# Kernel tuning notes

Measured on AMD Instinct MI355X. Metric: run time of the kernel, lower is better.

Reference implementation:

```python
import jax, jax.numpy as jnp
import numpy as np

H = 8  # attention_heads


def _ln(x, w, b, eps=1e-5):
    mu = x.mean(axis=-1, keepdims=True)
    var = x.var(axis=-1, keepdims=True)
    return (x - mu) / jnp.sqrt(var + eps) * w + b


def setup_inputs() -> dict:
    key = jax.random.key(0)
    ks = jax.random.split(key, 10)
    B, T, C, U, D, P = 4, 256, 2048, 4, 512, 512
    s = 0.02
    inp = {
        "model_embed": jax.random.normal(ks[0], (B, T, D), jnp.float32),
        "context_embed_key": jax.random.normal(ks[1], (C, U, D), jnp.float32),
        "context_embed_value": jax.random.normal(ks[2], (C, D), jnp.float32),
        "ln1_w": jnp.ones((D,), jnp.float32), "ln1_b": jnp.zeros((D,), jnp.float32),
        "ln2_w": jnp.ones((D,), jnp.float32), "ln2_b": jnp.zeros((D,), jnp.float32),
        "ln3_w": jnp.ones((D,), jnp.float32), "ln3_b": jnp.zeros((D,), jnp.float32),
        "ln4_w": jnp.ones((D,), jnp.float32), "ln4_b": jnp.zeros((D,), jnp.float32),
        "wq": jax.random.normal(ks[3], (D, D), jnp.float32) * s, "bq": jnp.zeros((D,), jnp.float32),
        "wk": jax.random.normal(ks[4], (D, D), jnp.float32) * s, "bk": jnp.zeros((D,), jnp.float32),
        "wv": jax.random.normal(ks[5], (D, D), jnp.float32) * s, "bv": jnp.zeros((D,), jnp.float32),
        "wo": jax.random.normal(ks[6], (D, D), jnp.float32) * s, "bo": jnp.zeros((D,), jnp.float32),
        "wp": jax.random.normal(ks[7], (D, P), jnp.float32) * s, "bp": jnp.zeros((P,), jnp.float32),
    }
    return inp


def reference(model_embed, context_embed_key, context_embed_value,
              ln1_w, ln1_b, ln2_w, ln2_b, ln3_w, ln3_b, ln4_w, ln4_b,
              wq, bq, wk, bk, wv, bv, wo, bo, wp, bp):
    B, T, D = model_embed.shape
    C, U, _ = context_embed_key.shape
    dk = D // H
    # pre-attention LayerNorms (norm_before_x1/x2/x3)
    q = _ln(model_embed, ln1_w, ln1_b)
    k = _ln(context_embed_key, ln2_w, ln2_b)
    v = _ln(context_embed_value, ln3_w, ln3_b)
    # q/k/v projections, split heads
    q = (q @ wq + bq).reshape(B, T, H, dk)
    k = (k @ wk + bk).reshape(C, U, H, dk)
    v = (v @ wv + bv).reshape(C, H, dk)
    # ColBERT late interaction: score every query token against every
    # context vector, MaxSim over the U vectors of each context entry.
    scores = jnp.einsum('bthd,cuhd->bhtcu', q, k) / jnp.sqrt(jnp.asarray(dk, q.dtype))
    scores = scores.max(axis=-1)                 # [B,H,T,C]
    attn = jax.nn.softmax(scores, axis=-1)       # softmax over contexts C
    out = jnp.einsum('bhtc,chd->bthd', attn, v).reshape(B, T, D)
    out = out @ wo + bo                          # attention output proj
    out = _ln(out, ln4_w, ln4_b)                 # norm_after
    return out @ wp + bp                         # final proj -> [B,T,P]
```

## Files before the change

kernel.cpp:

```cpp
#include <hip/hip_runtime.h>
#include <hip/hip_bf16.h>

using bf16 = __hip_bfloat16;

#define D_DIM 512
#define C_DIM 2048
#define U_DIM 4
#define DK 64

typedef __attribute__((ext_vector_type(8))) short short8;
typedef __attribute__((ext_vector_type(8))) unsigned short ushort8;
typedef __attribute__((ext_vector_type(4))) float f32x4;

__device__ __forceinline__ float dload(const void* p, size_t i, int f) {
    return f ? ((const float*)p)[i] : __bfloat162float(((const bf16*)p)[i]);
}
__device__ __forceinline__ unsigned f2bf(float x) {
    bf16 b = __float2bfloat16(x);
    return (unsigned)*(unsigned short*)&b;
}
__device__ __forceinline__ float bf2f(unsigned short us) {
    unsigned u = ((unsigned)us) << 16;
    return __builtin_bit_cast(float, u);
}

__device__ __forceinline__ int block_detect(const void* __restrict__ x) {
    __shared__ int sred[4];
    const bf16* xb = (const bf16*)x;
    int tid = threadIdx.x;
    int cnt = 0;
    #pragma unroll
    for (int i = 0; i < 4; ++i) {
        ushort8 a = *(const ushort8*)(xb + (size_t)(i * 256 + tid) * 8);
        #pragma unroll
        for (int j = 0; j < 8; ++j) {
            float v = fabsf(bf2f(a[j]));
            if (!(v <= 100.0f)) cnt++;
        }
    }
    #pragma unroll
    for (int o = 32; o > 0; o >>= 1) cnt += __shfl_down(cnt, o);
    if ((tid & 63) == 0) sred[tid >> 6] = cnt;
    __syncthreads();
    int c = sred[0] + sred[1] + sred[2] + sred[3];
    return (c > 400) ? 1 : 0;
}

template <bool LN, bool XF, bool WF>
__device__ __forceinline__ void pack_a_body(const void* __restrict__ X,
                                            const void* __restrict__ lnw,
                                            const void* __restrict__ lnb,
                                            uint4* __restrict__ Af, int tt) {
    int m = threadIdx.x >> 4;
    int kbL = threadIdx.x & 15;
    int row = tt * 16 + m;
    float v[32];
    float s = 0.0f, ss = 0.0f;
    #pragma unroll
    for (int i = 0; i < 4; ++i) {
        int k0 = (kbL + i * 16) * 8;
        if constexpr (XF) {
            const float4* p = (const float4*)((const float*)X + (size_t)row * D_DIM + k0);
            float4 a = p[0], b = p[1];
            v[i*8+0] = a.x; v[i*8+1] = a.y; v[i*8+2] = a.z; v[i*8+3] = a.w;
            v[i*8+4] = b.x; v[i*8+5] = b.y; v[i*8+6] = b.z; v[i*8+7] = b.w;
        } else {
            ushort8 a = *(const ushort8*)((const bf16*)X + (size_t)row * D_DIM + k0);
            #pragma unroll
            for (int j = 0; j < 8; ++j) v[i*8+j] = bf2f(a[j]);
        }
        #pragma unroll
        for (int j = 0; j < 8; ++j) { float x = v[i*8+j]; s += x; ss += x * x; }
    }
    float mu = 0.0f, rs = 1.0f;
    if (LN) {
        #pragma unroll
        for (int o = 1; o < 16; o <<= 1) { s += __shfl_xor(s, o); ss += __shfl_xor(ss, o); }
        mu = s * (1.0f / D_DIM);
        float var = ss * (1.0f / D_DIM) - mu * mu;
        rs = rsqrtf(var + 1e-5f);
    }
    #pragma unroll
    for (int i = 0; i < 4; ++i) {
        int kb = kbL + i * 16;
        int k0 = kb * 8;
        float lw[8], lb[8];
        if (LN) {
            if constexpr (WF) {
                const float4* pw = (const float4*)((const float*)lnw + k0);
                const float4* pb = (const float4*)((const float*)lnb + k0);
                float4 w0 = pw[0], w1 = pw[1], b0 = pb[0], b1 = pb[1];
                lw[0]=w0.x; lw[1]=w0.y; lw[2]=w0.z; lw[3]=w0.w;
                lw[4]=w1.x; lw[5]=w1.y; lw[6]=w1.z; lw[7]=w1.w;
                lb[0]=b0.x; lb[1]=b0.y; lb[2]=b0.z; lb[3]=b0.w;
                lb[4]=b1.x; lb[5]=b1.y; lb[6]=b1.z; lb[7]=b1.w;
            } else {
                ushort8 w8 = *(const ushort8*)((const bf16*)lnw + k0);
                ushort8 b8 = *(const ushort8*)((const bf16*)lnb + k0);
                #pragma unroll
                for (int j = 0; j < 8; ++j) { lw[j] = bf2f(w8[j]); lb[j] = bf2f(b8[j]); }
            }
        }
        unsigned pk[4];
        #pragma unroll
        for (int jp = 0; jp < 4; ++jp) {
            float v0 = v[i * 8 + jp * 2];
            float v1 = v[i * 8 + jp * 2 + 1];
            if (LN) {
                v0 = (v0 - mu) * rs * lw[jp * 2] + lb[jp * 2];
                v1 = (v1 - mu) * rs * lw[jp * 2 + 1] + lb[jp * 2 + 1];
            }
            pk[jp] = f2bf(v0) | (f2bf(v1) << 16);
        }
        uint4 wv = {pk[0], pk[1], pk[2], pk[3]};
        Af[((size_t)tt * 64 + kb) * 16 + m] = wv;
    }
}

template <bool WF>
__device__ __forceinline__ void pack_w_body(const void* __restrict__ W,
                                            uint4* __restrict__ Bf, int b,
                                            float (*t)[65]) {
    int n0 = (b & 7) * 64, k0 = (b >> 3) * 64;
    int tid = threadIdx.x;
    if constexpr (WF) {
        #pragma unroll
        for (int i = 0; i < 4; ++i) {
            int e = i * 256 + tid;
            int r = e >> 4, c = (e & 15) * 4;
            float4 a = *(const float4*)((const float*)W + (size_t)(k0 + r) * D_DIM + n0 + c);
            t[r][c] = a.x; t[r][c+1] = a.y; t[r][c+2] = a.z; t[r][c+3] = a.w;
        }
    } else {
        #pragma unroll
        for (int i = 0; i < 2; ++i) {
            int e = i * 256 + tid;
            int r = e >> 3, c = (e & 7) * 8;
            ushort8 a = *(const ushort8*)((const bf16*)W + (size_t)(k0 + r) * D_DIM + n0 + c);
            #pragma unroll
            for (int j = 0; j < 8; ++j) t[r][c + j] = bf2f(a[j]);
        }
    }
    __syncthreads();
    #pragma unroll
    for (int i = 0; i < 2; ++i) {
        int e = i * 256 + tid;
        int nl = e & 63, kbl = e >> 6;
        unsigned pk[4];
        #pragma unroll
        for (int jp = 0; jp < 4; ++jp)
            pk[jp] = f2bf(t[kbl * 8 + jp * 2][nl]) | (f2bf(t[kbl * 8 + jp * 2 + 1][nl]) << 16);
        uint4 wv = {pk[0], pk[1], pk[2], pk[3]};
        int n = n0 + nl;
        Bf[(((size_t)(n >> 4)) * 64 + (k0 / 8 + kbl)) * 16 + (n & 15)] = wv;
    }
}

__global__ __launch_bounds__(256, 1)
void pack_all_kernel(const void* __restrict__ me, const void* __restrict__ l1w, const void* __restrict__ l1b,
                     const void* __restrict__ ck, const void* __restrict__ l2w, const void* __restrict__ l2b,
                     const void* __restrict__ cv, const void* __restrict__ l3w, const void* __restrict__ l3b,
                     uint4* __restrict__ Aq, uint4* __restrict__ Ak, uint4* __restrict__ Av,
                     const void* W0, const void* W1, const void* W2,
                     const void* W3, const void* W4,
                     uint4* B0, uint4* B1, uint4* B2, uint4* B3, uint4* B4,
                     int* __restrict__ flagp) {
    __shared__ float t[64][65];
    int f = block_detect(me);
    if (blockIdx.x == 0 && threadIdx.x == 0) *flagp = f;
    int b = blockIdx.x;
    const void* Ws[5] = {W0, W1, W2, W3, W4};
    uint4* Bs[5] = {B0, B1, B2, B3, B4};
    if (f) {
        if (b < 64)       pack_a_body<true, true, true>(me, l1w, l1b, Aq, b);
        else if (b < 576) pack_a_body<true, true, true>(ck, l2w, l2b, Ak, b - 64);
        else if (b < 704) pack_a_body<true, true, true>(cv, l3w, l3b, Av, b - 576);
        else { int c = b - 704; pack_w_body<true>(Ws[c >> 6], Bs[c >> 6], c & 63, t); }
    } else {
        if (b < 64)       pack_a_body<true, false, false>(me, l1w, l1b, Aq, b);
        else if (b < 576) pack_a_body<true, false, false>(ck, l2w, l2b, Ak, b - 64);
        else if (b < 704) pack_a_body<true, false, false>(cv, l3w, l3b, Av, b - 576);
        else { int c = b - 704; pack_w_body<false>(Ws[c >> 6], Bs[c >> 6], c & 63, t); }
    }
}

template <int OUT>
__device__ __forceinline__ void mfma_gemm_body(const uint4* __restrict__ Af,
                                               const uint4* __restrict__ Bf,
                                               const void* __restrict__ bias,
                                               uint4* __restrict__ Fout, int Rtt,
                                               int f, int bx, int by,
                                               float (*t)[65]) {
    int w = threadIdx.x >> 6, lane = threadIdx.x & 63;
    int q = lane >> 4, mn = lane & 15;
    int mt = by * 4 + w;
    int nt0 = bx * 4;
    f32x4 acc[4] = {{0.f,0.f,0.f,0.f},{0.f,0.f,0.f,0.f},{0.f,0.f,0.f,0.f},{0.f,0.f,0.f,0.f}};
    for (int kw = 0; kw < 16; ++kw) {
        short8 a = *(const short8*)(Af + ((size_t)mt * 64 + kw * 4 + q) * 16 + mn);
        #pragma unroll
        for (int i = 0; i < 4; ++i) {
            short8 b = *(const short8*)(Bf + (((size_t)(nt0 + i)) * 64 + kw * 4 + q) * 16 + mn);
            acc[i] = __builtin_amdgcn_mfma_f32_16x16x32_bf16(a, b, acc[i], 0, 0, 0);
        }
    }
    #pragma unroll
    for (int i = 0; i < 4; ++i) {
        float bv = dload(bias, (nt0 + i) * 16 + mn, f);
        #pragma unroll
        for (int r = 0; r < 4; ++r)
            t[w * 16 + q * 4 + r][i * 16 + mn] = acc[i][r] + bv;
    }
    __syncthreads();
    int h = bx;
    if constexpr (OUT == 1) {
        #pragma unroll
        for (int e0 = 0; e0 < 2; ++e0) {
            int e = e0 * 256 + threadIdx.x;
            int m = e & 15, kb = (e >> 4) & 7, ttl = e >> 7;
            const float* src = &t[ttl * 16 + m][kb * 8];
            uint4 wv;
            wv.x = f2bf(src[0]) | (f2bf(src[1]) << 16);
            wv.y = f2bf(src[2]) | (f2bf(src[3]) << 16);
            wv.z = f2bf(src[4]) | (f2bf(src[5]) << 16);
            wv.w = f2bf(src[6]) | (f2bf(src[7]) << 16);
            Fout[(((size_t)h * Rtt + by * 4 + ttl) * 8 + kb) * 16 + m] = wv;
        }
    } else if constexpr (OUT == 2) {
        #pragma unroll
        for (int e0 = 0; e0 < 2; ++e0) {
            int e = e0 * 256 + threadIdx.x;
            int lane2 = e & 63, nt = (e >> 6) & 3, ctl = e >> 8;
            int nm2 = lane2 & 15, q2 = lane2 >> 4;
            int col = nt * 16 + nm2;
            int rb = ctl * 32 + q2 * 8;
            uint4 wv;
            wv.x = f2bf(t[rb + 0][col]) | (f2bf(t[rb + 1][col]) << 16);
            wv.y = f2bf(t[rb + 2][col]) | (f2bf(t[rb + 3][col]) << 16);
            wv.z = f2bf(t[rb + 4][col]) | (f2bf(t[rb + 5][col]) << 16);
            wv.w = f2bf(t[rb + 6][col]) | (f2bf(t[rb + 7][col]) << 16);
            Fout[(((size_t)h * 64 + by * 2 + ctl) * 4 + nt) * 64 + lane2] = wv;
        }
    } else {
        #pragma unroll
        for (int e0 = 0; e0 < 2; ++e0) {
            int e = e0 * 256 + threadIdx.x;
            int m2 = e & 15, kb = (e >> 4) & 7, u = e >> 7;
            const float* src = &t[m2 * 4 + u][kb * 8];
            uint4 wv;
            wv.x = f2bf(src[0]) | (f2bf(src[1]) << 16);
            wv.y = f2bf(src[2]) | (f2bf(src[3]) << 16);
            wv.z = f2bf(src[4]) | (f2bf(src[5]) << 16);
            wv.w = f2bf(src[6]) | (f2bf(src[7]) << 16);
            int nt = by * 4 + u;
            Fout[(((size_t)h * 512 + nt) * 8 + kb) * 16 + m2] = wv;
        }
    }
}

__global__ __launch_bounds__(256, 1)
void gemm_qkv_kernel(const uint4* __restrict__ Aq, const uint4* __restrict__ Ak,
                     const uint4* __restrict__ Av,
                     const uint4* __restrict__ wfq, const uint4* __restrict__ wfk,
                     const uint4* __restrict__ wfv,
                     const void* __restrict__ bq, const void* __restrict__ bk,
                     const void* __restrict__ bv,
                     uint4* __restrict__ qf, uint4* __restrict__ kf,
                     uint4* __restrict__ vf,
                     const int* __restrict__ flagp) {
    __shared__ float t[64][65];
    int f = *flagp;
    int b = blockIdx.x;
    if (b < 1024) {
        mfma_gemm_body<3>(Ak, wfk, bk, kf, 512, f, b & 7, b >> 3, t);
    } else if (b < 1280) {
        int c = b - 1024;
        mfma_gemm_body<2>(Av, wfv, bv, vf, 0, f, c & 7, c >> 3, t);
    } else {
        int c = b - 1280;
        mfma_gemm_body<1>(Aq, wfq, bq, qf, 64, f, c & 7, c >> 3, t);
    }
}

__global__ __launch_bounds__(256, 1)
void attn_fused_kernel(const uint4* __restrict__ qf, const uint4* __restrict__ kf,
                       const uint4* __restrict__ vf,
                       float* __restrict__ pacc, float* __restrict__ pm,
                       float* __restrict__ pl) {
    __shared__ float sp[4][16][36];
    int tid = threadIdx.x;
    int w = tid >> 6, lane = tid & 63;
    int q = lane >> 4, nm = lane & 15;
    int b = blockIdx.x;
    int s = b & 7;
    int h = (b >> 3) & 7;
    int qb = b >> 6;
    int mt = qb * 4 + w;

    short8 a0 = *(const short8*)(qf + (((size_t)h * 64 + mt) * 8 + q) * 16 + nm);
    short8 a1 = *(const short8*)(qf + (((size_t)h * 64 + mt) * 8 + 4 + q) * 16 + nm);

    f32x4 sc[8][2];
    #pragma unroll
    for (int st = 0; st < 8; ++st) {
        #pragma unroll
        for (int hh = 0; hh < 2; ++hh) {
            int ct16 = (s * 8 + st) * 2 + hh;
            f32x4 scv = {-1e30f, -1e30f, -1e30f, -1e30f};
            __builtin_amdgcn_s_setprio(1);
            #pragma unroll
            for (int u = 0; u < 4; ++u) {
                int nt = ct16 * 4 + u;
                short8 b0 = *(const short8*)(kf + (((size_t)h * 512 + nt) * 8 + q) * 16 + nm);
                short8 b1 = *(const short8*)(kf + (((size_t)h * 512 + nt) * 8 + 4 + q) * 16 + nm);
                f32x4 acc = {0.0f, 0.0f, 0.0f, 0.0f};
                acc = __builtin_amdgcn_mfma_f32_16x16x32_bf16(a0, b0, acc, 0, 0, 0);
                acc = __builtin_amdgcn_mfma_f32_16x16x32_bf16(a1, b1, acc, 0, 0, 0);
                #pragma unroll
                for (int r = 0; r < 4; ++r) scv[r] = fmaxf(scv[r], acc[r]);
            }
            __builtin_amdgcn_s_setprio(0);
            #pragma unroll
            for (int r = 0; r < 4; ++r) sc[st][hh][r] = scv[r] * 0.125f;
        }
    }

    float mrow[4], lrow[4];
    #pragma unroll
    for (int r = 0; r < 4; ++r) {
        float m = sc[0][0][r];
        #pragma unroll
        for (int st = 0; st < 8; ++st) {
            m = fmaxf(m, sc[st][0][r]);
            m = fmaxf(m, sc[st][1][r]);
        }
        m = fmaxf(m, __shfl_xor(m, 1));
        m = fmaxf(m, __shfl_xor(m, 2));
        m = fmaxf(m, __shfl_xor(m, 4));
        m = fmaxf(m, __shfl_xor(m, 8));
        mrow[r] = m;
        lrow[r] = 0.0f;
    }

    f32x4 acc_o[4] = {{0.f,0.f,0.f,0.f},{0.f,0.f,0.f,0.f},{0.f,0.f,0.f,0.f},{0.f,0.f,0.f,0.f}};
    #pragma unroll
    for (int st = 0; st < 8; ++st) {
        #pragma unroll
        for (int r = 0; r < 4; ++r) {
            float p0 = __expf(sc[st][0][r] - mrow[r]);
            float p1 = __expf(sc[st][1][r] - mrow[r]);
            sp[w][q * 4 + r][nm] = p0;
            sp[w][q * 4 + r][16 + nm] = p1;
            lrow[r] += p0 + p1;
        }
        float4 pa0 = *(const float4*)&sp[w][nm][q * 8];
        float4 pa1 = *(const float4*)&sp[w][nm][q * 8 + 4];
        uint4 av;
        av.x = f2bf(pa0.x) | (f2bf(pa0.y) << 16);
        av.y = f2bf(pa0.z) | (f2bf(pa0.w) << 16);
        av.z = f2bf(pa1.x) | (f2bf(pa1.y) << 16);
        av.w = f2bf(pa1.z) | (f2bf(pa1.w) << 16);
        short8 ap = *(short8*)&av;
        int ct32 = s * 8 + st;
        __builtin_amdgcn_s_setprio(1);
        #pragma unroll
        for (int nt2 = 0; nt2 < 4; ++nt2) {
            short8 bv = *(const short8*)(vf + (((size_t)h * 64 + ct32) * 4 + nt2) * 64 + lane);
            acc_o[nt2] = __builtin_amdgcn_mfma_f32_16x16x32_bf16(ap, bv, acc_o[nt2], 0, 0, 0);
        }
        __builtin_amdgcn_s_setprio(0);
    }

    #pragma unroll
    for (int r = 0; r < 4; ++r) {
        float ps = lrow[r];
        ps += __shfl_xor(ps, 1);
        ps += __shfl_xor(ps, 2);
        ps += __shfl_xor(ps, 4);
        ps += __shfl_xor(ps, 8);
        lrow[r] = ps;
    }

    int p_idx = ((qb * 8 + h) << 3) + s;
    float* po = pacc + ((size_t)p_idx * 64 + w * 16) * 64;
    #pragma unroll
    for (int nt2 = 0; nt2 < 4; ++nt2)
        #pragma unroll
        for (int r = 0; r < 4; ++r)
            po[(q * 4 + r) * 64 + nt2 * 16 + nm] = acc_o[nt2][r];
    if (nm == 0) {
        #pragma unroll
        for (int r = 0; r < 4; ++r) {
            pm[p_idx * 64 + w * 16 + q * 4 + r] = mrow[r];
            pl[p_idx * 64 + w * 16 + q * 4 + r] = lrow[r];
        }
    }
}

__global__ __launch_bounds__(256, 1)
void tail_kernel(const float* __restrict__ pacc, const float* __restrict__ pm,
                 const float* __restrict__ pl,
                 const uint4* __restrict__ wfo, const uint4* __restrict__ wfp,
                 const void* __restrict__ bo, const void* __restrict__ bp,
                 const void* __restrict__ ln4w, const void* __restrict__ ln4b,
                 float* __restrict__ Y, const int* __restrict__ flagp) {
    __shared__ uint4 lfr[64][16];
    __shared__ float xs[4][16][132];
    __shared__ float lw4[512], lb4[512];
    __shared__ float sred[4][16][2];
    int f = *flagp;
    int tid = threadIdx.x;
    int rt = blockIdx.x;
    int qb = rt >> 2;
    int row64base = (rt & 3) * 16;

    for (int i = tid; i < 512; i += 256) { lw4[i] = dload(ln4w, i, f); lb4[i] = dload(ln4b, i, f); }

    {
        int row16 = tid >> 4;
        int seg   = tid & 15;
        int h = seg >> 1, half = seg & 1;
        int t_loc = row64base + row16;
        int p0 = (qb * 8 + h) << 3;
        float M = -1e30f;
        #pragma unroll
        for (int s = 0; s < 8; ++s) M = fmaxf(M, pm[(p0 + s) * 64 + t_loc]);
        float L = 0.0f;
        float4 o[8] = {};
        #pragma unroll
        for (int s = 0; s < 8; ++s) {
            float e = __expf(pm[(p0 + s) * 64 + t_loc] - M);
            L += pl[(p0 + s) * 64 + t_loc] * e;
            const float4* po = (const float4*)(pacc + ((size_t)(p0 + s) * 64 + t_loc) * 64 + half * 32);
            #pragma unroll
            for (int d = 0; d < 8; ++d) {
                float4 v = po[d];
                o[d].x += v.x * e; o[d].y += v.y * e; o[d].z += v.z * e; o[d].w += v.w * e;
            }
        }
        float inv = 1.0f / L;
        #pragma unroll
        for (int j = 0; j < 4; ++j) {
            uint4 u;
            u.x = f2bf(o[j*2].x * inv)   | (f2bf(o[j*2].y * inv) << 16);
            u.y = f2bf(o[j*2].z * inv)   | (f2bf(o[j*2].w * inv) << 16);
            u.z = f2bf(o[j*2+1].x * inv) | (f2bf(o[j*2+1].y * inv) << 16);
            u.w = f2bf(o[j*2+1].z * inv) | (f2bf(o[j*2+1].w * inv) << 16);
            lfr[h * 8 + half * 4 + j][row16] = u;
        }
    }
    __syncthreads();

    int w = tid >> 6, lane = tid & 63;
    int q = lane >> 4, mn = lane & 15;
    f32x4 acc[8];
    #pragma unroll
    for (int i = 0; i < 8; ++i) acc[i] = {0.f, 0.f, 0.f, 0.f};
    for (int kw = 0; kw < 16; ++kw) {
        short8 a = *(const short8*)&lfr[kw * 4 + q][mn];
        #pragma unroll
        for (int i = 0; i < 8; ++i) {
            int nt = w * 8 + i;
            short8 b = *(const short8*)(wfo + ((size_t)nt * 64 + kw * 4 + q) * 16 + mn);
            acc[i] = __builtin_amdgcn_mfma_f32_16x16x32_bf16(a, b, acc[i], 0, 0, 0);
        }
    }
    #pragma unroll
    for (int i = 0; i < 8; ++i) {
        float bv = dload(bo, (w * 8 + i) * 16 + mn, f);
        #pragma unroll
        for (int r = 0; r < 4; ++r) acc[i][r] += bv;
    }

    {
        float ps[4], pq[4];
        #pragma unroll
        for (int r = 0; r < 4; ++r) {
            float s = 0.f, sq = 0.f;
            #pragma unroll
            for (int i = 0; i < 8; ++i) { float x = acc[i][r]; s += x; sq += x * x; }
            #pragma unroll
            for (int o = 1; o < 16; o <<= 1) { s += __shfl_xor(s, o); sq += __shfl_xor(sq, o); }
            ps[r] = s; pq[r] = sq;
        }
        if (mn == 0) {
            #pragma unroll
            for (int r = 0; r < 4; ++r) { sred[w][q*4+r][0] = ps[r]; sred[w][q*4+r][1] = pq[r]; }
        }
    }
    __syncthreads();

    float mu[4], rs[4];
    #pragma unroll
    for (int r = 0; r < 4; ++r) {
        int rr = q * 4 + r;
        float s  = sred[0][rr][0] + sred[1][rr][0] + sred[2][rr][0] + sred[3][rr][0];
        float sq = sred[0][rr][1] + sred[1][rr][1] + sred[2][rr][1] + sred[3][rr][1];
        mu[r] = s * (1.0f / D_DIM);
        float var = sq * (1.0f / D_DIM) - mu[r] * mu[r];
        rs[r] = rsqrtf(var + 1e-5f);
    }

    #pragma unroll
    for (int i = 0; i < 8; ++i) {
        int col = w * 128 + i * 16 + mn;
        float g = lw4[col], bb = lb4[col];
        #pragma unroll
        for (int r = 0; r < 4; ++r) {
            float x = (acc[i][r] - mu[r]) * rs[r] * g + bb;
            xs[w][q * 4 + r][i * 16 + mn] = x;
        }
    }
    __syncthreads();

    #pragma unroll
    for (int it = 0; it < 4; ++it) {
        int m = mn;
        int kbl = q + it * 4;
        const float* src = &xs[w][m][kbl * 8];
        float4 s0 = *(const float4*)src;
        float4 s1 = *(const float4*)(src + 4);
        uint4 u;
        u.x = f2bf(s0.x) | (f2bf(s0.y) << 16);
        u.y = f2bf(s0.z) | (f2bf(s0.w) << 16);
        u.z = f2bf(s1.x) | (f2bf(s1.y) << 16);
        u.w = f2bf(s1.z) | (f2bf(s1.w) << 16);
        lfr[w * 16 + kbl][m] = u;
    }
    __syncthreads();

    f32x4 acc2[8];
    #pragma unroll
    for (int i = 0; i < 8; ++i) acc2[i] = {0.f, 0.f, 0.f, 0.f};
    for (int kw = 0; kw < 16; ++kw) {
        short8 a = *(const short8*)&lfr[kw * 4 + q][mn];
        #pragma unroll
        for (int i = 0; i < 8; ++i) {
            int nt = w * 8 + i;
            short8 b = *(const short8*)(wfp + ((size_t)nt * 64 + kw * 4 + q) * 16 + mn);
            acc2[i] = __builtin_amdgcn_mfma_f32_16x16x32_bf16(a, b, acc2[i], 0, 0, 0);
        }
    }
    #pragma unroll
    for (int i = 0; i < 8; ++i) {
        int col = w * 128 + i * 16 + mn;
        float bv = dload(bp, col, f);
        #pragma unroll
        for (int r = 0; r < 4; ++r)
            Y[(size_t)(rt * 16 + q * 4 + r) * D_DIM + col] = acc2[i][r] + bv;
    }
}

extern "C" void kernel_launch(void* const* d_in, const int* in_sizes, int n_in,
                              void* d_out, int out_size, void* d_ws, size_t ws_size,
                              hipStream_t stream) {
    const void* model_embed = d_in[0];
    const void* ctx_key     = d_in[1];
    const void* ctx_val     = d_in[2];
    const void* ln1w = d_in[3];  const void* ln1b = d_in[4];
    const void* ln2w = d_in[5];  const void* ln2b = d_in[6];
    const void* ln3w = d_in[7];  const void* ln3b = d_in[8];
    const void* ln4w = d_in[9];  const void* ln4b = d_in[10];
    const void* wq = d_in[11];   const void* bq = d_in[12];
    const void* wk = d_in[13];   const void* bk = d_in[14];
    const void* wv = d_in[15];   const void* bv = d_in[16];
    const void* wo = d_in[17];   const void* bo = d_in[18];
    const void* wp = d_in[19];   const void* bp = d_in[20];

    int*   flagp = (int*)d_ws;
    float* ws    = (float*)d_ws + 16;
    float* o1    = ws;
    float* qTf   = o1 + 524288;
    float* kTf   = qTf + 262144;
    float* Aqf   = kTf + 2097152;
    float* Akf   = Aqf + 262144;
    float* Avf   = Akf + 2097152;
    float* vff   = Avf + 524288;
    float* pacc2 = vff + 524288;
    float* pm2   = pacc2 + 4194304;
    float* pl2   = pm2 + 65536;
    float* wfr   = pl2 + 65536;

    uint4* qf  = (uint4*)qTf;
    uint4* kf  = (uint4*)kTf;
    uint4* Aq  = (uint4*)Aqf;
    uint4* Ak  = (uint4*)Akf;
    uint4* Av  = (uint4*)Avf;
    uint4* vf  = (uint4*)vff;
    uint4* wfq = (uint4*)wfr;
    uint4* wfk = wfq + 32768;
    uint4* wfv = wfk + 32768;
    uint4* wfo = wfv + 32768;
    uint4* wfp = wfo + 32768;

    pack_all_kernel<<<1024, 256, 0, stream>>>(model_embed, ln1w, ln1b,
                                              ctx_key, ln2w, ln2b,
                                              ctx_val, ln3w, ln3b,
                                              Aq, Ak, Av,
                                              wq, wk, wv, wo, wp,
                                              wfq, wfk, wfv, wfo, wfp, flagp);

    gemm_qkv_kernel<<<1408, 256, 0, stream>>>(Aq, Ak, Av, wfq, wfk, wfv,
                                              bq, bk, bv, qf, kf, vf, flagp);

    attn_fused_kernel<<<1024, 256, 0, stream>>>(qf, kf, vf, pacc2, pm2, pl2);

    tail_kernel<<<64, 256, 0, stream>>>(pacc2, pm2, pl2, wfo, wfp,
                                        bo, bp, ln4w, ln4b,
                                        (float*)d_out, flagp);

    (void)ws_size;
}
```

Baseline: 207.7 us.

## Split attention merge into separate kernel and widen tail blocks; reorder block indices

Moves the split-softmax merge of partial attention outputs out of the 64-block tail kernel into its own 256-block kernel, which writes bf16 MFMA fragments to workspace. The tail kernel now uses 512 threads with 8 waves, each computing 4 column tiles instead of 8. Block index mappings in the QKV GEMM and attention kernels are also reordered, presumably to improve locality of K/V tile reuse across concurrently running blocks. The intent is to spread the memory-bound merge across more CUs, at the cost of an extra launch and a global round-trip for the merged output.

```diff
diff --git a/kernel.cpp b/kernel.cpp
--- a/kernel.cpp
+++ b/kernel.cpp
@@ -272,13 +272,13 @@
     int f = *flagp;
     int b = blockIdx.x;
     if (b < 1024) {
-        mfma_gemm_body<3>(Ak, wfk, bk, kf, 512, f, b & 7, b >> 3, t);
+        mfma_gemm_body<3>(Ak, wfk, bk, kf, 512, f, b >> 7, b & 127, t);
     } else if (b < 1280) {
         int c = b - 1024;
-        mfma_gemm_body<2>(Av, wfv, bv, vf, 0, f, c & 7, c >> 3, t);
+        mfma_gemm_body<2>(Av, wfv, bv, vf, 0, f, c >> 5, c & 31, t);
     } else {
         int c = b - 1280;
-        mfma_gemm_body<1>(Aq, wfq, bq, qf, 64, f, c & 7, c >> 3, t);
+        mfma_gemm_body<1>(Aq, wfq, bq, qf, 64, f, c >> 4, c & 15, t);
     }
 }
 
@@ -292,8 +292,8 @@
     int w = tid >> 6, lane = tid & 63;
     int q = lane >> 4, nm = lane & 15;
     int b = blockIdx.x;
-    int s = b & 7;
-    int h = (b >> 3) & 7;
+    int h = b & 7;
+    int s = (b >> 3) & 7;
     int qb = b >> 6;
     int mt = qb * 4 + w;
 
@@ -398,76 +398,72 @@
 }
 
 __global__ __launch_bounds__(256, 1)
-void tail_kernel(const float* __restrict__ pacc, const float* __restrict__ pm,
-                 const float* __restrict__ pl,
-                 const uint4* __restrict__ wfo, const uint4* __restrict__ wfp,
-                 const void* __restrict__ bo, const void* __restrict__ bp,
-                 const void* __restrict__ ln4w, const void* __restrict__ ln4b,
-                 float* __restrict__ Y, const int* __restrict__ flagp) {
+void attn_merge_kernel(const float* __restrict__ pacc, const float* __restrict__ pm,
+                       const float* __restrict__ pl, uint4* __restrict__ oAf) {
+    int b = blockIdx.x;
+    int g = b >> 1;
+    int qb = g >> 3, h = g & 7;
+    int tid = threadIdx.x;
+    int r32 = tid >> 3, dg = tid & 7;
+    int t_loc = (b & 1) * 32 + r32;
+    int p0 = g * 8;
+    float M = -1e30f;
+    #pragma unroll
+    for (int s = 0; s < 8; ++s) M = fmaxf(M, pm[(p0 + s) * 64 + t_loc]);
+    float L = 0.0f;
+    float4 o0 = {}, o1 = {};
+    #pragma unroll
+    for (int s = 0; s < 8; ++s) {
+        float e = __expf(pm[(p0 + s) * 64 + t_loc] - M);
+        L += pl[(p0 + s) * 64 + t_loc] * e;
+        const float4* po = (const float4*)(pacc + ((size_t)(p0 + s) * 64 + t_loc) * 64 + dg * 8);
+        float4 v0 = po[0], v1 = po[1];
+        o0.x += v0.x * e; o0.y += v0.y * e; o0.z += v0.z * e; o0.w += v0.w * e;
+        o1.x += v1.x * e; o1.y += v1.y * e; o1.z += v1.z * e; o1.w += v1.w * e;
+    }
+    float inv = 1.0f / L;
+    int t = qb * 64 + t_loc;
+    int tt = t >> 4, m = t & 15;
+    int kb = h * 8 + dg;
+    uint4 u;
+    u.x = f2bf(o0.x * inv) | (f2bf(o0.y * inv) << 16);
+    u.y = f2bf(o0.z * inv) | (f2bf(o0.w * inv) << 16);
+    u.z = f2bf(o1.x * inv) | (f2bf(o1.y * inv) << 16);
+    u.w = f2bf(o1.z * inv) | (f2bf(o1.w * inv) << 16);
+    oAf[((size_t)tt * 64 + kb) * 16 + m] = u;
+}
+
+__global__ __launch_bounds__(512, 1)
+void tail2_kernel(const uint4* __restrict__ oAf,
+                  const uint4* __restrict__ wfo, const uint4* __restrict__ wfp,
+                  const void* __restrict__ bo, const void* __restrict__ bp,
+                  const void* __restrict__ ln4w, const void* __restrict__ ln4b,
+                  float* __restrict__ Y, const int* __restrict__ flagp) {
     __shared__ uint4 lfr[64][16];
-    __shared__ float xs[4][16][132];
+    __shared__ float xs[8][16][68];
     __shared__ float lw4[512], lb4[512];
-    __shared__ float sred[4][16][2];
+    __shared__ float sred[8][16][2];
     int f = *flagp;
     int tid = threadIdx.x;
     int rt = blockIdx.x;
-    int qb = rt >> 2;
-    int row64base = (rt & 3) * 16;
-
-    for (int i = tid; i < 512; i += 256) { lw4[i] = dload(ln4w, i, f); lb4[i] = dload(ln4b, i, f); }
-
-    {
-        int row16 = tid >> 4;
-        int seg   = tid & 15;
-        int h = seg >> 1, half = seg & 1;
-        int t_loc = row64base + row16;
-        int p0 = (qb * 8 + h) << 3;
-        float M = -1e30f;
-        #pragma unroll
-        for (int s = 0; s < 8; ++s) M = fmaxf(M, pm[(p0 + s) * 64 + t_loc]);
-        float L = 0.0f;
-        float4 o[8] = {};
-        #pragma unroll
-        for (int s = 0; s < 8; ++s) {
-            float e = __expf(pm[(p0 + s) * 64 + t_loc] - M);
-            L += pl[(p0 + s) * 64 + t_loc] * e;
-            const float4* po = (const float4*)(pacc + ((size_t)(p0 + s) * 64 + t_loc) * 64 + half * 32);
-            #pragma unroll
-            for (int d = 0; d < 8; ++d) {
-                float4 v = po[d];
-                o[d].x += v.x * e; o[d].y += v.y * e; o[d].z += v.z * e; o[d].w += v.w * e;
-            }
-        }
-        float inv = 1.0f / L;
-        #pragma unroll
-        for (int j = 0; j < 4; ++j) {
-            uint4 u;
-            u.x = f2bf(o[j*2].x * inv)   | (f2bf(o[j*2].y * inv) << 16);
-            u.y = f2bf(o[j*2].z * inv)   | (f2bf(o[j*2].w * inv) << 16);
-            u.z = f2bf(o[j*2+1].x * inv) | (f2bf(o[j*2+1].y * inv) << 16);
-            u.w = f2bf(o[j*2+1].z * inv) | (f2bf(o[j*2+1].w * inv) << 16);
-            lfr[h * 8 + half * 4 + j][row16] = u;
-        }
-    }
-    __syncthreads();
+    if (tid < 512) { lw4[tid] = dload(ln4w, tid, f); lb4[tid] = dload(ln4b, tid, f); }
 
     int w = tid >> 6, lane = tid & 63;
     int q = lane >> 4, mn = lane & 15;
-    f32x4 acc[8];
-    #pragma unroll
-    for (int i = 0; i < 8; ++i) acc[i] = {0.f, 0.f, 0.f, 0.f};
+
+    f32x4 acc[4] = {{0.f,0.f,0.f,0.f},{0.f,0.f,0.f,0.f},{0.f,0.f,0.f,0.f},{0.f,0.f,0.f,0.f}};
     for (int kw = 0; kw < 16; ++kw) {
-        short8 a = *(const short8*)&lfr[kw * 4 + q][mn];
-        #pragma unroll
-        for (int i = 0; i < 8; ++i) {
-            int nt = w * 8 + i;
+        short8 a = *(const short8*)(oAf + ((size_t)rt * 64 + kw * 4 + q) * 16 + mn);
+        #pragma unroll
+        for (int i = 0; i < 4; ++i) {
+            int nt = w * 4 + i;
             short8 b = *(const short8*)(wfo + ((size_t)nt * 64 + kw * 4 + q) * 16 + mn);
             acc[i] = __builtin_amdgcn_mfma_f32_16x16x32_bf16(a, b, acc[i], 0, 0, 0);
         }
     }
     #pragma unroll
-    for (int i = 0; i < 8; ++i) {
-        float bv = dload(bo, (w * 8 + i) * 16 + mn, f);
+    for (int i = 0; i < 4; ++i) {
+        float bv = dload(bo, (w * 4 + i) * 16 + mn, f);
         #pragma unroll
         for (int r = 0; r < 4; ++r) acc[i][r] += bv;
     }
@@ -478,7 +474,7 @@
         for (int r = 0; r < 4; ++r) {
             float s = 0.f, sq = 0.f;
             #pragma unroll
-            for (int i = 0; i < 8; ++i) { float x = acc[i][r]; s += x; sq += x * x; }
+            for (int i = 0; i < 4; ++i) { float x = acc[i][r]; s += x; sq += x * x; }
             #pragma unroll
             for (int o = 1; o < 16; o <<= 1) { s += __shfl_xor(s, o); sq += __shfl_xor(sq, o); }
             ps[r] = s; pq[r] = sq;
@@ -494,16 +490,17 @@
     #pragma unroll
     for (int r = 0; r < 4; ++r) {
         int rr = q * 4 + r;
-        float s  = sred[0][rr][0] + sred[1][rr][0] + sred[2][rr][0] + sred[3][rr][0];
-        float sq = sred[0][rr][1] + sred[1][rr][1] + sred[2][rr][1] + sred[3][rr][1];
+        float s = 0.f, sq = 0.f;
+        #pragma unroll
+        for (int ww = 0; ww < 8; ++ww) { s += sred[ww][rr][0]; sq += sred[ww][rr][1]; }
         mu[r] = s * (1.0f / D_DIM);
         float var = sq * (1.0f / D_DIM) - mu[r] * mu[r];
         rs[r] = rsqrtf(var + 1e-5f);
     }
 
     #pragma unroll
-    for (int i = 0; i < 8; ++i) {
-        int col = w * 128 + i * 16 + mn;
+    for (int i = 0; i < 4; ++i) {
+        int col = w * 64 + i * 16 + mn;
         float g = lw4[col], bb = lb4[col];
         #pragma unroll
         for (int r = 0; r < 4; ++r) {
@@ -514,9 +511,9 @@
     __syncthreads();
 
     #pragma unroll
-    for (int it = 0; it < 4; ++it) {
-        int m = mn;
-        int kbl = q + it * 4;
+    for (int it = 0; it < 2; ++it) {
+        int idx = it * 64 + lane;
+        int m = idx & 15, kbl = idx >> 4;
         const float* src = &xs[w][m][kbl * 8];
         float4 s0 = *(const float4*)src;
         float4 s1 = *(const float4*)(src + 4);
@@ -525,25 +522,23 @@
         u.y = f2bf(s0.z) | (f2bf(s0.w) << 16);
         u.z = f2bf(s1.x) | (f2bf(s1.y) << 16);
         u.w = f2bf(s1.z) | (f2bf(s1.w) << 16);
-        lfr[w * 16 + kbl][m] = u;
+        lfr[w * 8 + kbl][m] = u;
     }
     __syncthreads();
 
-    f32x4 acc2[8];
-    #pragma unroll
-    for (int i = 0; i < 8; ++i) acc2[i] = {0.f, 0.f, 0.f, 0.f};
+    f32x4 acc2[4] = {{0.f,0.f,0.f,0.f},{0.f,0.f,0.f,0.f},{0.f,0.f,0.f,0.f},{0.f,0.f,0.f,0.f}};
     for (int kw = 0; kw < 16; ++kw) {
         short8 a = *(const short8*)&lfr[kw * 4 + q][mn];
         #pragma unroll
-        for (int i = 0; i < 8; ++i) {
-            int nt = w * 8 + i;
+        for (int i = 0; i < 4; ++i) {
+            int nt = w * 4 + i;
             short8 b = *(const short8*)(wfp + ((size_t)nt * 64 + kw * 4 + q) * 16 + mn);
             acc2[i] = __builtin_amdgcn_mfma_f32_16x16x32_bf16(a, b, acc2[i], 0, 0, 0);
         }
     }
     #pragma unroll
-    for (int i = 0; i < 8; ++i) {
-        int col = w * 128 + i * 16 + mn;
+    for (int i = 0; i < 4; ++i) {
+        int col = (w * 4 + i) * 16 + mn;
         float bv = dload(bp, col, f);
         #pragma unroll
         for (int r = 0; r < 4; ++r)
@@ -587,6 +582,7 @@
     uint4* Ak  = (uint4*)Akf;
     uint4* Av  = (uint4*)Avf;
     uint4* vf  = (uint4*)vff;
+    uint4* oAf = (uint4*)o1;
     uint4* wfq = (uint4*)wfr;
     uint4* wfk = wfq + 32768;
     uint4* wfv = wfk + 32768;
@@ -605,9 +601,10 @@
 
     attn_fused_kernel<<<1024, 256, 0, stream>>>(qf, kf, vf, pacc2, pm2, pl2);
 
-    tail_kernel<<<64, 256, 0, stream>>>(pacc2, pm2, pl2, wfo, wfp,
-                                        bo, bp, ln4w, ln4b,
-                                        (float*)d_out, flagp);
+    attn_merge_kernel<<<256, 256, 0, stream>>>(pacc2, pm2, pl2, oAf);
+
+    tail2_kernel<<<64, 512, 0, stream>>>(oAf, wfo, wfp, bo, bp,
+                                         ln4w, ln4b, (float*)d_out, flagp);
 
     (void)ws_size;
 }
```

New measurement: 185.9 us. -10.5%, faster.
